# Kernel optimization log

Hardware: AMD Instinct MI355X
Metric: run time of the kernel (lower is better)

Reference implementation:

```python
import jax, jax.numpy as jnp
import numpy as np

B = 32768
S = 1024          # max_seq_len
DF = 0.99         # discount_factor
AL = 0.95         # advantage_lambda


def _grad_scale(x, s):
    # forward: identity; backward: grad * s (mirrors GradScaler.apply)
    return s * x + jax.lax.stop_gradient((1.0 - s) * x)


def setup_inputs() -> dict:
    key = jax.random.key(0)
    k1, k2 = jax.random.split(key, 2)
    values = jax.random.normal(k1, (B, S + 1, 1), dtype=jnp.float32)
    rewards = jax.random.normal(k2, (B, S, 1), dtype=jnp.float32)
    dones = jnp.zeros((B, S, 1), dtype=jnp.float32)
    raw_gamma = jnp.zeros((1,), dtype=jnp.float32)
    raw_lambd = jnp.zeros((S,), dtype=jnp.float32)
    return {"values": values, "rewards": rewards, "dones": dones,
            "raw_gamma": raw_gamma, "raw_lambd": raw_lambd}


def reference(values, rewards, dones, raw_gamma, raw_lambd):
    # dynamic gamma (scalar) and per-timestep lambda, as in the properties
    gamma = _grad_scale(DF + (1.0 - DF) * (2.0 * jax.nn.sigmoid(raw_gamma) - 1.0), 1.0)[0]
    lam = _grad_scale(AL + (1.0 - AL) * (2.0 * jax.nn.sigmoid(raw_lambd) - 1.0), 0.5)  # [S]

    # time-major views for the scan: [S, B, 1]
    r_tm = jnp.swapaxes(rewards, 0, 1)
    d_tm = jnp.swapaxes(dones, 0, 1)
    v_next_tm = jnp.swapaxes(values[:, 1:], 0, 1)  # values[:, t+1]

    init = (jnp.zeros_like(values[:, -1]), values[:, -1])  # (sum_rewards[S], lambda_returns[S]=values[:, -1])

    def step(carry, xs):
        sr_next, lr_next = carry
        r_t, d_t, v_t, lam_t = xs
        g = gamma * (1.0 - d_t)
        # sum_rewards computed under no_grad in the original
        sr = jax.lax.stop_gradient(r_t + g * (lam_t * sr_next))
        lr = r_t + g * ((1.0 - lam_t) * v_t + lam_t * lr_next)
        return (sr, lr), (sr, lr)

    # backward recurrence over time; outputs returned in forward time order
    _, (sum_r_tm, lam_ret_tm) = jax.lax.scan(step, init, (r_tm, d_tm, v_next_tm, lam), reverse=True)

    lambda_returns = jnp.swapaxes(lam_ret_tm, 0, 1)  # [B, S, 1] == original [:, :-1]
    sum_rewards = jnp.swapaxes(sum_r_tm, 0, 1)       # [B, S, 1]
    return lambda_returns, sum_rewards
```

## Files before the change

### kernel.cpp

```cpp
#include <hip/hip_runtime.h>
#include <math.h>


#define DF_C 0.99f
#define AL_C 0.95f

__global__ __launch_bounds__(256) void td_scan_kernel(
    const float* __restrict__ values,
    const float* __restrict__ rewards,
    const float* __restrict__ dones,
    const float* __restrict__ raw_gamma,
    const float* __restrict__ raw_lambd,
    float* __restrict__ out,
    int B, int S)
{
    const int b   = blockIdx.x;
    const int tid = threadIdx.x;
    const int t0  = tid * 4;

    const float rg    = raw_gamma[0];
    const float sg    = 1.0f / (1.0f + expf(-rg));
    const float gamma = DF_C + (1.0f - DF_C) * (2.0f * sg - 1.0f);

    const size_t rbase = (size_t)b * S + t0;
    const float4 r4 = *reinterpret_cast<const float4*>(rewards + rbase);
    const float4 d4 = *reinterpret_cast<const float4*>(dones   + rbase);
    float r[4] = {r4.x, r4.y, r4.z, r4.w};
    float d[4] = {d4.x, d4.y, d4.z, d4.w};

    const float* vrow = values + (size_t)b * (S + 1);
    float v[4], lam[4];
#pragma unroll
    for (int j = 0; j < 4; ++j) {
        v[j] = vrow[t0 + j + 1];
        const float x = raw_lambd[t0 + j];
        const float s = 1.0f / (1.0f + expf(-x));
        lam[j] = AL_C + (1.0f - AL_C) * (2.0f * s - 1.0f);
    }

    float Al = 0.0f, As = 0.0f, Bp = 1.0f;
#pragma unroll
    for (int j = 0; j < 4; ++j) {
        const float g  = gamma * (1.0f - d[j]);
        const float bt = g * lam[j];
        const float at = r[j] + g * (1.0f - lam[j]) * v[j];
        Al = Al + Bp * at;
        As = As + Bp * r[j];
        Bp = Bp * bt;
    }

    __shared__ float sAl[256], sAs[256], sB[256];
    sAl[tid] = Al; sAs[tid] = As; sB[tid] = Bp;
    __syncthreads();
#pragma unroll
    for (int off = 1; off < 256; off <<= 1) {
        float al = 0.0f, as_ = 0.0f, bb = 1.0f;
        const bool valid = (tid + off) < 256;
        if (valid) { al = sAl[tid + off]; as_ = sAs[tid + off]; bb = sB[tid + off]; }
        __syncthreads();
        if (valid) {
            const float mb = sB[tid];
            sAl[tid] = sAl[tid] + mb * al;
            sAs[tid] = sAs[tid] + mb * as_;
            sB[tid]  = mb * bb;
        }
        __syncthreads();
    }

    float Aex_l = 0.0f, Aex_s = 0.0f, Bex = 1.0f;
    if (tid < 255) { Aex_l = sAl[tid + 1]; Aex_s = sAs[tid + 1]; Bex = sB[tid + 1]; }

    const float v_last = vrow[S];
    float lr = Aex_l + Bex * v_last;
    float sr = Aex_s;

    float out_lr[4], out_sr[4];
#pragma unroll
    for (int j = 3; j >= 0; --j) {
        const float g  = gamma * (1.0f - d[j]);
        const float bt = g * lam[j];
        sr = r[j] + bt * sr;
        lr = r[j] + g * (1.0f - lam[j]) * v[j] + bt * lr;
        out_lr[j] = lr;
        out_sr[j] = sr;
    }

    *reinterpret_cast<float4*>(out + rbase) =
        make_float4(out_lr[0], out_lr[1], out_lr[2], out_lr[3]);
    *reinterpret_cast<float4*>(out + (size_t)B * S + rbase) =
        make_float4(out_sr[0], out_sr[1], out_sr[2], out_sr[3]);
}

extern "C" void kernel_launch(void* const* d_in, const int* in_sizes, int n_in,
                              void* d_out, int out_size, void* d_ws, size_t ws_size,
                              hipStream_t stream) {
    const float* values    = (const float*)d_in[0];
    const float* rewards   = (const float*)d_in[1];
    const float* dones     = (const float*)d_in[2];
    const float* raw_gamma = (const float*)d_in[3];
    const float* raw_lambd = (const float*)d_in[4];
    float* out = (float*)d_out;

    const int S = in_sizes[4];
    const int B = in_sizes[1] / S;

    dim3 grid(B);
    dim3 block(S / 4);
    td_scan_kernel<<<grid, block, 0, stream>>>(values, rewards, dones,
                                               raw_gamma, raw_lambd, out, B, S);
}
```

Measured before the change: 510.1 us.

## Replace shared-memory block scan with wavefront shuffle scan plus cross-wave combine

Replaces the 256-thread Hillis-Steele scan over shared memory, which needed two barriers per step, with a 64-lane shuffle-based suffix scan inside each wavefront. Four per-wave totals are then combined through a small shared array behind a single barrier. The value loads are also folded into one 16-byte memcpy, but that load is misaligned because of the +1 offset. The change also leaves an empty dead loop in the code.

```diff
diff --git a/kernel.cpp b/kernel.cpp
--- a/kernel.cpp
+++ b/kernel.cpp
@@ -14,9 +14,11 @@
     float* __restrict__ out,
     int B, int S)
 {
-    const int b   = blockIdx.x;
-    const int tid = threadIdx.x;
-    const int t0  = tid * 4;
+    const int b    = blockIdx.x;
+    const int tid  = threadIdx.x;
+    const int lane = tid & 63;
+    const int wv   = tid >> 6;
+    const int t0   = tid * 4;
 
     const float rg    = raw_gamma[0];
     const float sg    = 1.0f / (1.0f + expf(-rg));
@@ -29,10 +31,13 @@
     float d[4] = {d4.x, d4.y, d4.z, d4.w};
 
     const float* vrow = values + (size_t)b * (S + 1);
-    float v[4], lam[4];
+    float v[4];
+    __builtin_memcpy(v, vrow + t0 + 1, 16);
+    const float v_last = vrow[S];
+
+    float lam[4];
 #pragma unroll
     for (int j = 0; j < 4; ++j) {
-        v[j] = vrow[t0 + j + 1];
         const float x = raw_lambd[t0 + j];
         const float s = 1.0f / (1.0f + expf(-x));
         lam[j] = AL_C + (1.0f - AL_C) * (2.0f * s - 1.0f);
@@ -49,30 +54,39 @@
         Bp = Bp * bt;
     }
 
-    __shared__ float sAl[256], sAs[256], sB[256];
-    sAl[tid] = Al; sAs[tid] = As; sB[tid] = Bp;
-    __syncthreads();
 #pragma unroll
-    for (int off = 1; off < 256; off <<= 1) {
-        float al = 0.0f, as_ = 0.0f, bb = 1.0f;
-        const bool valid = (tid + off) < 256;
-        if (valid) { al = sAl[tid + off]; as_ = sAs[tid + off]; bb = sB[tid + off]; }
-        __syncthreads();
-        if (valid) {
-            const float mb = sB[tid];
-            sAl[tid] = sAl[tid] + mb * al;
-            sAs[tid] = sAs[tid] + mb * as_;
-            sB[tid]  = mb * bb;
+    for (int off = 1; off < 64; off <<= 1) {
+        const float al  = __shfl_down(Al, off);
+        const float as_ = __shfl_down(As, off);
+        const float bb  = __shfl_down(Bp, off);
+        if (lane + off < 64) {
+            Al = Al + Bp * al;
+            As = As + Bp * as_;
+            Bp = Bp * bb;
         }
-        __syncthreads();
     }
 
-    float Aex_l = 0.0f, Aex_s = 0.0f, Bex = 1.0f;
-    if (tid < 255) { Aex_l = sAl[tid + 1]; Aex_s = sAs[tid + 1]; Bex = sB[tid + 1]; }
+    float eAl = __shfl_down(Al, 1);
+    float eAs = __shfl_down(As, 1);
+    float eB  = __shfl_down(Bp, 1);
+    if (lane == 63) { eAl = 0.0f; eAs = 0.0f; eB = 1.0f; }
 
-    const float v_last = vrow[S];
-    float lr = Aex_l + Bex * v_last;
-    float sr = Aex_s;
+    __shared__ float wA_l[4], wA_s[4], wB_[4];
+    if (lane == 0) { wA_l[wv] = Al; wA_s[wv] = As; wB_[wv] = Bp; }
+    __syncthreads();
+
+#pragma unroll
+    for (int w2 = 1; w2 < 4; ++w2) {
+        if (w2 > wv + 0 && (wv + (4 - w2)) < 4) {  }
+    }
+    for (int w2 = wv + 1; w2 < 4; ++w2) {
+        eAl = eAl + eB * wA_l[w2];
+        eAs = eAs + eB * wA_s[w2];
+        eB  = eB  * wB_[w2];
+    }
+
+    float lr = eAl + eB * v_last;
+    float sr = eAs;
 
     float out_lr[4], out_sr[4];
 #pragma unroll
```

Result: no change. 508.5 us (-0.3%).
